# Kernel optimization log

Measured on AMD Instinct MI355X. Metric: run time of the kernel, lower is better.

Reference implementation:

```python
import jax, jax.numpy as jnp
import numpy as np

N = 4
SEGMENTS = 16
IN_F = 256
OUT_F = 256
BATCH = 512


def chebyshev_lobatto(n):
    # Chebyshev-Lobatto interpolation nodes on [-1, 1]
    k = jnp.arange(n, dtype=jnp.float32)
    return -jnp.cos(jnp.pi * k / (n - 1))


def lagrange_basis(x, nodes):
    # x: [B, In]; returns basis values [B, In, n]
    n = nodes.shape[0]
    cols = []
    for j in range(n):  # n is a small static constant (4)
        terms = [(x - nodes[m]) / (nodes[j] - nodes[m]) for m in range(n) if m != j]
        cols.append(jnp.prod(jnp.stack(terms, axis=0), axis=0))
    return jnp.stack(cols, axis=-1)


def setup_inputs() -> dict:
    key = jax.random.key(0)
    k1, k2 = jax.random.split(key)
    x = jax.random.uniform(k1, (BATCH, IN_F), dtype=jnp.float32, minval=-1.0, maxval=1.0)
    w = jax.random.uniform(
        k2, (OUT_F, IN_F, (N - 1) * SEGMENTS + 1), dtype=jnp.float32, minval=-1.0, maxval=1.0
    )
    return {"x": x, "w": w, "n": N, "segments": SEGMENTS}


def reference(x, w, n, segments):
    nodes = chebyshev_lobatto(n)
    # segment id per element, clamped to [0, segments-1]
    id_min = jnp.clip(((x + 1.0) / 2.0 * segments).astype(jnp.int32), 0, segments - 1)
    id_max = id_min + 1
    wid_min = id_min * (n - 1)  # start of weight slice; slice length == n
    # segment boundaries in x-space: eta(i) = i/segments * 2 - 1
    x_min = id_min.astype(x.dtype) / segments * 2.0 - 1.0
    x_max = id_max.astype(x.dtype) / segments * 2.0 - 1.0
    # rescale x into [-1, 1] within its segment
    x_in = 2.0 * (x - x_min) / (x_max - x_min) - 1.0
    basis = lagrange_basis(x_in, nodes)  # [B, In, n]
    # gather per-element weight slice: w_g[b,i,j,o] = w[o, i, wid_min[b,i]+j]
    idx = wid_min[..., None] + jnp.arange(n)  # [B, In, n]
    w_t = jnp.transpose(w, (1, 2, 0))  # [In, K, Out]
    in_f = w.shape[1]
    w_g = w_t[jnp.arange(in_f)[None, :, None], idx]  # [B, In, n, Out]
    # interpolate and sum over in_features (matches einsum 'ijk,jkli->jl')
    return jnp.einsum("bin,bino->bo", basis, w_g)
```

## Files before the change

kernel.cpp:

```cpp
#include <hip/hip_runtime.h>


#define INF     256
#define OUTF    256
#define WSTRIDE 49
#define OSTRIDE (INF * WSTRIDE)

#define GLOAD_LDS(gptr, lptr)                                                       \
  __builtin_amdgcn_global_load_lds(                                                 \
      (const __attribute__((address_space(1))) unsigned int*)(gptr),                \
      (__attribute__((address_space(3))) unsigned int*)(lptr), 4, 0, 0)

__global__ __launch_bounds__(256, 1)
void pp_kernel(const float* __restrict__ x, const float* __restrict__ w,
               float* __restrict__ out) {
    __shared__ float smem[32768];

    const int tid  = threadIdx.x;
    const int wave = tid >> 6;
    const int lane = tid & 63;
    const int i_base = blockIdx.x * 8;
    const int o_base = blockIdx.y * 64;
    const int b_base = blockIdx.z * 256;
    const int b_me   = b_base + tid;

    float c[8][4];
    int   sseg[8];
    {
        const float4* xp = (const float4*)(x + (size_t)b_me * INF + i_base);
        float4 xv0 = xp[0], xv1 = xp[1];
        float xs[8] = {xv0.x, xv0.y, xv0.z, xv0.w, xv1.x, xv1.y, xv1.z, xv1.w};
        #pragma unroll
        for (int i = 0; i < 8; ++i) {
            float xx = xs[i];
            int id = (int)((xx + 1.0f) * 8.0f);
            id = id < 0 ? 0 : (id > 15 ? 15 : id);
            float u = (xx - ((float)id * 0.125f - 1.0f)) * 16.0f - 1.0f;
            float a = u + 1.0f, b2 = u + 0.5f, cc = u - 0.5f, d = u - 1.0f;
            c[i][0] = b2 * cc * d * (-2.0f / 3.0f);
            c[i][1] = a  * cc * d * ( 4.0f / 3.0f);
            c[i][2] = a  * b2 * d * (-4.0f / 3.0f);
            c[i][3] = a  * b2 * cc * ( 2.0f / 3.0f);
            sseg[i] = id;
        }
    }

    const int lane_t = 3 * (lane >> 2) + (lane & 3);

    #define STAGE(ci)                                                                 \
    do {                                                                              \
        const int bufd_ = (ci & 1) * 16384;                                           \
        for (int t = 0; t < 64; ++t) {                                                \
            int r = t * 4 + wave;                   \
            int i_loc = r >> 6, o = r & 63;                                           \
            const float* gp = w + (size_t)(o_base + o) * OSTRIDE                      \
                                + (i_base + (ci) * 4 + i_loc) * WSTRIDE + lane_t;     \
            GLOAD_LDS(gp, &smem[bufd_ + r * 64]);                                     \
        }                                                                             \
    } while (0)

    float acc[64];
    #pragma unroll
    for (int o = 0; o < 64; ++o) acc[o] = 0.0f;

    #define COMPUTE(ci)                                                               \
    do {                                                                              \
        const float* p0 = &smem[(ci & 1) * 16384 +     0 + sseg[(ci)*4 + 0] * 4];     \
        const float* p1 = &smem[(ci & 1) * 16384 +  4096 + sseg[(ci)*4 + 1] * 4];     \
        const float* p2 = &smem[(ci & 1) * 16384 +  8192 + sseg[(ci)*4 + 2] * 4];     \
        const float* p3 = &smem[(ci & 1) * 16384 + 12288 + sseg[(ci)*4 + 3] * 4];     \
        _Pragma("unroll")                                                             \
        for (int o = 0; o < 64; ++o) {                                                \
            float4 w0 = *(const float4*)(p0 + o * 64);                                \
            float4 w1 = *(const float4*)(p1 + o * 64);                                \
            float4 w2 = *(const float4*)(p2 + o * 64);                                \
            float4 w3 = *(const float4*)(p3 + o * 64);                                \
            float t0 = acc[o];                                                        \
            t0 += c[(ci)*4+0][0]*w0.x; t0 += c[(ci)*4+0][1]*w0.y;                     \
            t0 += c[(ci)*4+0][2]*w0.z; t0 += c[(ci)*4+0][3]*w0.w;                     \
            t0 += c[(ci)*4+1][0]*w1.x; t0 += c[(ci)*4+1][1]*w1.y;                     \
            t0 += c[(ci)*4+1][2]*w1.z; t0 += c[(ci)*4+1][3]*w1.w;                     \
            t0 += c[(ci)*4+2][0]*w2.x; t0 += c[(ci)*4+2][1]*w2.y;                     \
            t0 += c[(ci)*4+2][2]*w2.z; t0 += c[(ci)*4+2][3]*w2.w;                     \
            t0 += c[(ci)*4+3][0]*w3.x; t0 += c[(ci)*4+3][1]*w3.y;                     \
            t0 += c[(ci)*4+3][2]*w3.z; t0 += c[(ci)*4+3][3]*w3.w;                     \
            acc[o] = t0;                                                              \
        }                                                                             \
    } while (0)

    STAGE(0);
    __syncthreads();
    STAGE(1);
    COMPUTE(0);
    __syncthreads();
    COMPUTE(1);
    __syncthreads();

    #pragma unroll
    for (int o = 0; o < 64; ++o) smem[tid * 65 + o] = acc[o];
    __syncthreads();

    const int bg = b_base + wave * 64;
    for (int r = 0; r < 64; ++r) {
        float v = smem[(wave * 64 + r) * 65 + lane];
        atomicAdd(&out[(size_t)(bg + r) * OUTF + o_base + lane], v);
    }

    #undef STAGE
    #undef COMPUTE
}

extern "C" void kernel_launch(void* const* d_in, const int* in_sizes, int n_in,
                              void* d_out, int out_size, void* d_ws, size_t ws_size,
                              hipStream_t stream) {
    const float* x = (const float*)d_in[0];
    const float* w = (const float*)d_in[1];
    float* out = (float*)d_out;
    (void)d_ws; (void)ws_size; (void)n_in; (void)in_sizes;

    hipMemsetAsync(out, 0, (size_t)out_size * sizeof(float), stream);

    dim3 grid(32, 4, 2);
    pp_kernel<<<grid, 256, 0, stream>>>(x, w, out);
}
```

Measured before the change: 97.28 us.

## Replace atomic accumulation with split-K workspace partials and a separate reduce kernel

The fused kernel used a memset plus per-element atomicAdd to combine partial sums across input-feature splits. It is replaced by a partial kernel that writes per-split results to a workspace and a second kernel that sums the 32 splits. The partial kernel now handles 128 batch rows per block (grid 32x4x4) with each wave covering half the outputs, uses a smaller LDS footprint so two blocks fit per CU, and stages four double-buffered chunks of two input features. In exchange it writes and reads back 16 MB of workspace traffic and adds a second kernel launch.

```diff
diff --git a/kernel.cpp b/kernel.cpp
--- a/kernel.cpp
+++ b/kernel.cpp
@@ -6,108 +6,107 @@
 #define WSTRIDE 49
 #define OSTRIDE (INF * WSTRIDE)
 
+#define NSPLIT  32
+#define IPB     8
+#define ICH     2
+
 #define GLOAD_LDS(gptr, lptr)                                                       \
   __builtin_amdgcn_global_load_lds(                                                 \
       (const __attribute__((address_space(1))) unsigned int*)(gptr),                \
       (__attribute__((address_space(3))) unsigned int*)(lptr), 4, 0, 0)
 
-__global__ __launch_bounds__(256, 1)
-void pp_kernel(const float* __restrict__ x, const float* __restrict__ w,
-               float* __restrict__ out) {
-    __shared__ float smem[32768];
+#define STAGE(ci)                                                                   \
+do {                                                                                \
+    float* lbase_ = &smem[((ci) & 1) * 8192];                                       \
+    _Pragma("unroll")                                                               \
+    for (int t = 0; t < 32; ++t) {                                                  \
+        int r_ = t * 4 + wave;                              \
+        int i_loc_ = r_ >> 6, o_ = r_ & 63;                                         \
+        const float* gp_ = w + (size_t)(o_base + o_) * OSTRIDE                      \
+                             + (i_base + (ci) * ICH + i_loc_) * WSTRIDE + lane_t;   \
+        GLOAD_LDS(gp_, lbase_ + r_ * 64);                                           \
+    }                                                                               \
+} while (0)
+
+#define COMPUTE(ci)                                                                 \
+do {                                                                                \
+    _Pragma("unroll")                                                               \
+    for (int il = 0; il < ICH; ++il) {                                              \
+        const int ig_ = (ci) * ICH + il;                                            \
+        const float* p_ = &smem[((ci) & 1) * 8192 +                                 \
+                                (il * 64 + oh * 32) * 64 + sseg[ig_] * 4];          \
+        const float c0_ = c[ig_][0], c1_ = c[ig_][1];                               \
+        const float c2_ = c[ig_][2], c3_ = c[ig_][3];                               \
+        _Pragma("unroll")                                                           \
+        for (int oo = 0; oo < 32; ++oo) {                                           \
+            float4 wv_ = *(const float4*)(p_ + oo * 64);                            \
+            acc[oo] += c0_ * wv_.x + c1_ * wv_.y + c2_ * wv_.z + c3_ * wv_.w;       \
+        }                                                                           \
+    }                                                                               \
+} while (0)
+
+__global__ __launch_bounds__(256, 2)
+void pp_partial(const float* __restrict__ x, const float* __restrict__ w,
+                float* __restrict__ ws) {
+    __shared__ float smem[16384];
 
     const int tid  = threadIdx.x;
-    const int wave = tid >> 6;
-    const int lane = tid & 63;
-    const int i_base = blockIdx.x * 8;
+    const int wave = tid >> 6, lane = tid & 63;
+    const int isplit = blockIdx.x;
+    const int i_base = isplit * IPB;
     const int o_base = blockIdx.y * 64;
-    const int b_base = blockIdx.z * 256;
-    const int b_me   = b_base + tid;
+    const int b_base = blockIdx.z * 128;
+    const int bh = wave >> 1, oh = wave & 1;
+    const int b  = b_base + bh * 64 + lane;
+    const int lane_t = 3 * (lane >> 2) + (lane & 3);
 
-    float c[8][4];
-    int   sseg[8];
+    float c[IPB][4];
+    int   sseg[IPB];
     {
-        const float4* xp = (const float4*)(x + (size_t)b_me * INF + i_base);
-        float4 xv0 = xp[0], xv1 = xp[1];
-        float xs[8] = {xv0.x, xv0.y, xv0.z, xv0.w, xv1.x, xv1.y, xv1.z, xv1.w};
+        const float4* xp = (const float4*)(x + (size_t)b * INF + i_base);
+        float4 x0 = xp[0], x1 = xp[1];
+        float xs[8] = {x0.x, x0.y, x0.z, x0.w, x1.x, x1.y, x1.z, x1.w};
         #pragma unroll
-        for (int i = 0; i < 8; ++i) {
+        for (int i = 0; i < IPB; ++i) {
             float xx = xs[i];
             int id = (int)((xx + 1.0f) * 8.0f);
             id = id < 0 ? 0 : (id > 15 ? 15 : id);
             float u = (xx - ((float)id * 0.125f - 1.0f)) * 16.0f - 1.0f;
             float a = u + 1.0f, b2 = u + 0.5f, cc = u - 0.5f, d = u - 1.0f;
-            c[i][0] = b2 * cc * d * (-2.0f / 3.0f);
-            c[i][1] = a  * cc * d * ( 4.0f / 3.0f);
-            c[i][2] = a  * b2 * d * (-4.0f / 3.0f);
+            c[i][0] = b2 * cc * d  * (-2.0f / 3.0f);
+            c[i][1] = a  * cc * d  * ( 4.0f / 3.0f);
+            c[i][2] = a  * b2 * d  * (-4.0f / 3.0f);
             c[i][3] = a  * b2 * cc * ( 2.0f / 3.0f);
             sseg[i] = id;
         }
     }
 
-    const int lane_t = 3 * (lane >> 2) + (lane & 3);
-
-    #define STAGE(ci)                                                                 \
-    do {                                                                              \
-        const int bufd_ = (ci & 1) * 16384;                                           \
-        for (int t = 0; t < 64; ++t) {                                                \
-            int r = t * 4 + wave;                   \
-            int i_loc = r >> 6, o = r & 63;                                           \
-            const float* gp = w + (size_t)(o_base + o) * OSTRIDE                      \
-                                + (i_base + (ci) * 4 + i_loc) * WSTRIDE + lane_t;     \
-            GLOAD_LDS(gp, &smem[bufd_ + r * 64]);                                     \
-        }                                                                             \
-    } while (0)
-
-    float acc[64];
+    float acc[32];
     #pragma unroll
-    for (int o = 0; o < 64; ++o) acc[o] = 0.0f;
-
-    #define COMPUTE(ci)                                                               \
-    do {                                                                              \
-        const float* p0 = &smem[(ci & 1) * 16384 +     0 + sseg[(ci)*4 + 0] * 4];     \
-        const float* p1 = &smem[(ci & 1) * 16384 +  4096 + sseg[(ci)*4 + 1] * 4];     \
-        const float* p2 = &smem[(ci & 1) * 16384 +  8192 + sseg[(ci)*4 + 2] * 4];     \
-        const float* p3 = &smem[(ci & 1) * 16384 + 12288 + sseg[(ci)*4 + 3] * 4];     \
-        _Pragma("unroll")                                                             \
-        for (int o = 0; o < 64; ++o) {                                                \
-            float4 w0 = *(const float4*)(p0 + o * 64);                                \
-            float4 w1 = *(const float4*)(p1 + o * 64);                                \
-            float4 w2 = *(const float4*)(p2 + o * 64);                                \
-            float4 w3 = *(const float4*)(p3 + o * 64);                                \
-            float t0 = acc[o];                                                        \
-            t0 += c[(ci)*4+0][0]*w0.x; t0 += c[(ci)*4+0][1]*w0.y;                     \
-            t0 += c[(ci)*4+0][2]*w0.z; t0 += c[(ci)*4+0][3]*w0.w;                     \
-            t0 += c[(ci)*4+1][0]*w1.x; t0 += c[(ci)*4+1][1]*w1.y;                     \
-            t0 += c[(ci)*4+1][2]*w1.z; t0 += c[(ci)*4+1][3]*w1.w;                     \
-            t0 += c[(ci)*4+2][0]*w2.x; t0 += c[(ci)*4+2][1]*w2.y;                     \
-            t0 += c[(ci)*4+2][2]*w2.z; t0 += c[(ci)*4+2][3]*w2.w;                     \
-            t0 += c[(ci)*4+3][0]*w3.x; t0 += c[(ci)*4+3][1]*w3.y;                     \
-            t0 += c[(ci)*4+3][2]*w3.z; t0 += c[(ci)*4+3][3]*w3.w;                     \
-            acc[o] = t0;                                                              \
-        }                                                                             \
-    } while (0)
+    for (int q = 0; q < 32; ++q) acc[q] = 0.0f;
 
     STAGE(0);
     __syncthreads();
-    STAGE(1);
-    COMPUTE(0);
-    __syncthreads();
-    COMPUTE(1);
-    __syncthreads();
+    STAGE(1); COMPUTE(0); __syncthreads();
+    STAGE(2); COMPUTE(1); __syncthreads();
+    STAGE(3); COMPUTE(2); __syncthreads();
+    COMPUTE(3);
 
+    float4* wp = (float4*)(ws + (size_t)isplit * (512 * 256)
+                              + (size_t)b * 256 + o_base + oh * 32);
     #pragma unroll
-    for (int o = 0; o < 64; ++o) smem[tid * 65 + o] = acc[o];
-    __syncthreads();
+    for (int q = 0; q < 8; ++q)
+        wp[q] = make_float4(acc[4*q], acc[4*q+1], acc[4*q+2], acc[4*q+3]);
+}
 
-    const int bg = b_base + wave * 64;
-    for (int r = 0; r < 64; ++r) {
-        float v = smem[(wave * 64 + r) * 65 + lane];
-        atomicAdd(&out[(size_t)(bg + r) * OUTF + o_base + lane], v);
-    }
-
-    #undef STAGE
-    #undef COMPUTE
+__global__ __launch_bounds__(256)
+void pp_reduce(const float* __restrict__ ws, float* __restrict__ out) {
+    const size_t off = (size_t)blockIdx.x * 256 + threadIdx.x;
+    float s = 0.0f;
+    #pragma unroll
+    for (int k = 0; k < NSPLIT; ++k)
+        s += ws[(size_t)k * (512 * 256) + off];
+    out[off] = s;
 }
 
 extern "C" void kernel_launch(void* const* d_in, const int* in_sizes, int n_in,
@@ -116,10 +115,10 @@
     const float* x = (const float*)d_in[0];
     const float* w = (const float*)d_in[1];
     float* out = (float*)d_out;
-    (void)d_ws; (void)ws_size; (void)n_in; (void)in_sizes;
+    float* ws  = (float*)d_ws;
+    (void)ws_size; (void)n_in; (void)in_sizes; (void)out_size;
 
-    hipMemsetAsync(out, 0, (size_t)out_size * sizeof(float), stream);
-
-    dim3 grid(32, 4, 2);
-    pp_kernel<<<grid, 256, 0, stream>>>(x, w, out);
+    dim3 grid(NSPLIT, 4, 4);
+    pp_partial<<<grid, 256, 0, stream>>>(x, w, ws);
+    pp_reduce<<<dim3(512), 256, 0, stream>>>(ws, out);
 }
```

Result: faster. 87.87 us (-9.7%).
